# Kernel tuning notes

Hardware: AMD Instinct MI355X
Metric: run time of the kernel (lower is better)

Reference implementation:

```python
import jax, jax.numpy as jnp
import numpy as np

B, D, H, T = 4096, 64, 256, 200

def setup_inputs() -> dict:
    key = jax.random.key(0)
    ks = jax.random.split(key, 4)
    def xavier(k, fan_in, fan_out):
        lim = np.sqrt(6.0 / (fan_in + fan_out)).astype(np.float32)
        return jax.random.uniform(k, (fan_in, fan_out), jnp.float32, -lim, lim)
    return {
        "y0": jax.random.normal(ks[0], (B, D), jnp.float32),
        "t": jnp.arange(T, dtype=jnp.float32) * 0.01,
        "W1": xavier(ks[1], D, H),
        "b1": jnp.zeros((H,), jnp.float32),
        "W2": xavier(ks[2], H, H),
        "b2": jnp.zeros((H,), jnp.float32),
        "W3": xavier(ks[3], H, D),
        "b3": jnp.zeros((D,), jnp.float32),
    }

def reference(y0, t, W1, b1, W2, b2, W3, b3):
    # odeint uses constant dt = t[1] - t[0] (as in the original code)
    dt = t[1] - t[0]
    num_steps = t.shape[0]

    def mlp(y):  # dy/dt = f(y); autonomous, t unused
        h = jax.nn.relu(y @ W1 + b1)
        h = jax.nn.relu(h @ W2 + b2)
        return h @ W3 + b3

    def step(y, _):
        y_new = y + dt * mlp(y)
        return y_new, y_new

    _, ys = jax.lax.scan(step, y0, None, length=num_steps - 1)  # [T-1, B, D]
    # solution: [B, T, D] with solution[:, 0] = y0
    return jnp.concatenate([y0[:, None, :], jnp.transpose(ys, (1, 0, 2))], axis=1)
```

## Files before the change

kernel.cpp:

```cpp
#include <hip/hip_runtime.h>
#include <hip/hip_bf16.h>

#define BATCH   4096
#define DIM     64
#define HID     256
#define TSTEPS  200
#define SROWS   16
#define NBLOCKS (BATCH / SROWS)
#define NTH     512

#define HP  264
#define YPB 72

typedef __bf16 bf16_t;
typedef bf16_t bf16x8 __attribute__((ext_vector_type(8)));
typedef bf16_t bf16x2 __attribute__((ext_vector_type(2)));
typedef float  f32x4  __attribute__((ext_vector_type(4)));

__device__ __forceinline__ unsigned short f2bf(float f) {
    unsigned u = __builtin_bit_cast(unsigned, f);
    u += 0x7FFFu + ((u >> 16) & 1u);
    return (unsigned short)(u >> 16);
}

#if __has_builtin(__builtin_amdgcn_cvt_pk_bf16_f32)
__device__ __forceinline__ unsigned pk2(float lo, float hi) {
    return __builtin_bit_cast(unsigned, __builtin_amdgcn_cvt_pk_bf16_f32(lo, hi));
}
#else
__device__ __forceinline__ unsigned pk2(float lo, float hi) {
    return (unsigned)f2bf(lo) | ((unsigned)f2bf(hi) << 16);
}
#endif

__global__ void prep_weights(const float* __restrict__ W1,
                             const float* __restrict__ W2,
                             const float* __restrict__ W3,
                             unsigned short* __restrict__ ws) {
    int u = blockIdx.x * blockDim.x + threadIdx.x;
    if (u >= 12288) return;
    const int lane = u & 63, l16 = lane & 15, quad = lane >> 4;
    const float* src; int ld, m, k;
    if (u < 2048) {
        int r = u >> 6; int kk = r & 1; int mt = r >> 1;
        src = W1; ld = 256; m = mt * 16 + l16; k = kk * 32 + quad * 8;
    } else if (u < 10240) {
        int r = (u - 2048) >> 6; int kk = r & 7; int mt = r >> 3;
        src = W2; ld = 256; m = mt * 16 + l16; k = kk * 32 + quad * 8;
    } else {
        int r = (u - 10240) >> 6; int kk = r & 7; int mt = r >> 3;
        src = W3; ld = 64;  m = mt * 16 + l16; k = kk * 32 + quad * 8;
    }
    unsigned short tmp[8] __attribute__((aligned(16)));
    #pragma unroll
    for (int j = 0; j < 8; ++j)
        tmp[j] = f2bf(src[(size_t)(k + j) * ld + m]);
    *(uint4*)(ws + (size_t)u * 8) = *(const uint4*)tmp;
}

__global__ void __launch_bounds__(NTH, 2)
ode_kernel(const float* __restrict__ y0,
           const float* __restrict__ tarr,
           const float* __restrict__ b1,
           const float* __restrict__ b2,
           const float* __restrict__ b3,
           const unsigned short* __restrict__ wf,
           float* __restrict__ out) {
    __shared__ __align__(16) unsigned short ybt[SROWS * YPB];
    __shared__ __align__(16) unsigned short h1s[SROWS * HP];
    __shared__ __align__(16) unsigned short h2s[SROWS * HP];

    const int tid  = threadIdx.x;
    const int w    = tid >> 6;
    const int lane = tid & 63;
    const int l16  = lane & 15;
    const int quad = lane >> 4;
    const int b0   = blockIdx.x * SROWS;

    const float dt = tarr[1] - tarr[0];

    const bf16x8* wv = (const bf16x8*)wf;
    bf16x8 w1f[2][2], w2f[2][8], w3f[8];
    #pragma unroll
    for (int mt = 0; mt < 2; ++mt) {
        const int g = w * 2 + mt;
        #pragma unroll
        for (int kk = 0; kk < 2; ++kk) w1f[mt][kk] = wv[(g * 2 + kk) * 64 + lane];
        #pragma unroll
        for (int kk = 0; kk < 8; ++kk) w2f[mt][kk] = wv[2048 + (g * 8 + kk) * 64 + lane];
    }
    if (w < 4)
        #pragma unroll
        for (int kk = 0; kk < 8; ++kk) w3f[kk] = wv[10240 + (w * 8 + kk) * 64 + lane];

    f32x4 binit1[2], binit2[2], binit3;
    #pragma unroll
    for (int mt = 0; mt < 2; ++mt)
        #pragma unroll
        for (int r = 0; r < 4; ++r) {
            binit1[mt][r] = b1[w * 32 + mt * 16 + quad * 4 + r];
            binit2[mt][r] = b2[w * 32 + mt * 16 + quad * 4 + r];
        }

    float yreg[4];
    float* outp = out;
    if (w < 4) {
        #pragma unroll
        for (int r = 0; r < 4; ++r) binit3[r] = b3[w * 16 + quad * 4 + r];
        outp = out + (size_t)(b0 + l16) * (TSTEPS * DIM) + w * 16 + quad * 4;
        float4 v = *(const float4*)&y0[(size_t)(b0 + l16) * DIM + w * 16 + quad * 4];
        yreg[0] = v.x; yreg[1] = v.y; yreg[2] = v.z; yreg[3] = v.w;
        uint2 p; p.x = pk2(v.x, v.y); p.y = pk2(v.z, v.w);
        *(uint2*)&ybt[l16 * YPB + w * 16 + quad * 4] = p;
        *(float4*)outp = v;
        outp += DIM;
    }
    __syncthreads();

    const unsigned short* ybase  = &ybt[l16 * YPB];
    const unsigned short* h1base = &h1s[l16 * HP];
    const unsigned short* h2base = &h2s[l16 * HP];
    const int ep_off = l16 * HP + w * 32 + quad * 4;

    for (int t = 1; t < TSTEPS; ++t) {
        {
            f32x4 acc[2] = {binit1[0], binit1[1]};
            bf16x8 bfr[2];
            #pragma unroll
            for (int kk = 0; kk < 2; ++kk)
                bfr[kk] = *(const bf16x8*)&ybase[kk * 32 + quad * 8];
            #pragma unroll
            for (int kk = 0; kk < 2; ++kk)
                #pragma unroll
                for (int mt = 0; mt < 2; ++mt)
                    acc[mt] = __builtin_amdgcn_mfma_f32_16x16x32_bf16(
                        w1f[mt][kk], bfr[kk], acc[mt], 0, 0, 0);
            #pragma unroll
            for (int mt = 0; mt < 2; ++mt) {
                float v0 = acc[mt][0] > 0.f ? acc[mt][0] : 0.f;
                float v1 = acc[mt][1] > 0.f ? acc[mt][1] : 0.f;
                float v2 = acc[mt][2] > 0.f ? acc[mt][2] : 0.f;
                float v3 = acc[mt][3] > 0.f ? acc[mt][3] : 0.f;
                uint2 p; p.x = pk2(v0, v1); p.y = pk2(v2, v3);
                *(uint2*)&h1s[ep_off + mt * 16] = p;
            }
        }
        __syncthreads();

        {
            f32x4 acc[2] = {binit2[0], binit2[1]};
            bf16x8 bfr[8];
            #pragma unroll
            for (int kk = 0; kk < 8; ++kk)
                bfr[kk] = *(const bf16x8*)&h1base[kk * 32 + quad * 8];
            #pragma unroll
            for (int kk = 0; kk < 8; ++kk)
                #pragma unroll
                for (int mt = 0; mt < 2; ++mt)
                    acc[mt] = __builtin_amdgcn_mfma_f32_16x16x32_bf16(
                        w2f[mt][kk], bfr[kk], acc[mt], 0, 0, 0);
            #pragma unroll
            for (int mt = 0; mt < 2; ++mt) {
                float v0 = acc[mt][0] > 0.f ? acc[mt][0] : 0.f;
                float v1 = acc[mt][1] > 0.f ? acc[mt][1] : 0.f;
                float v2 = acc[mt][2] > 0.f ? acc[mt][2] : 0.f;
                float v3 = acc[mt][3] > 0.f ? acc[mt][3] : 0.f;
                uint2 p; p.x = pk2(v0, v1); p.y = pk2(v2, v3);
                *(uint2*)&h2s[ep_off + mt * 16] = p;
            }
        }
        __syncthreads();

        if (w < 4) {
            f32x4 acc = binit3;
            bf16x8 bfr[8];
            #pragma unroll
            for (int kk = 0; kk < 8; ++kk)
                bfr[kk] = *(const bf16x8*)&h2base[kk * 32 + quad * 8];
            #pragma unroll
            for (int kk = 0; kk < 8; ++kk)
                acc = __builtin_amdgcn_mfma_f32_16x16x32_bf16(
                    w3f[kk], bfr[kk], acc, 0, 0, 0);
            #pragma unroll
            for (int r = 0; r < 4; ++r)
                yreg[r] = __builtin_fmaf(dt, acc[r], yreg[r]);
            uint2 p; p.x = pk2(yreg[0], yreg[1]); p.y = pk2(yreg[2], yreg[3]);
            *(uint2*)&ybt[l16 * YPB + w * 16 + quad * 4] = p;
            float4 ov; ov.x = yreg[0]; ov.y = yreg[1]; ov.z = yreg[2]; ov.w = yreg[3];
            *(float4*)outp = ov;
            outp += DIM;
        }
        __syncthreads();
    }
}

extern "C" void kernel_launch(void* const* d_in, const int* in_sizes, int n_in,
                              void* d_out, int out_size, void* d_ws, size_t ws_size,
                              hipStream_t stream) {
    const float* y0 = (const float*)d_in[0];
    const float* t  = (const float*)d_in[1];
    const float* W1 = (const float*)d_in[2];
    const float* b1 = (const float*)d_in[3];
    const float* W2 = (const float*)d_in[4];
    const float* b2 = (const float*)d_in[5];
    const float* W3 = (const float*)d_in[6];
    const float* b3 = (const float*)d_in[7];
    float* out = (float*)d_out;
    unsigned short* wf = (unsigned short*)d_ws;

    prep_weights<<<48, 256, 0, stream>>>(W1, W2, W3, wf);
    ode_kernel<<<NBLOCKS, NTH, 0, stream>>>(y0, t, b1, b2, b3, wf, out);
}
```

Before: 382.8 us.

## Halve block to 4 waves, each owning 4 M-tiles; split layer-3 accumulation chains

Cuts the block from 8 to 4 wavefronts, so each wave computes four 16-row output tiles per layer instead of two, and all waves take part in layer 3 instead of only half. Layer 3's eight chained MFMAs are split into two independent accumulators to shorten the dependency chain. __syncthreads is replaced by a custom LDS-wait-plus-barrier. The aim is cheaper barriers and better MFMA pipelining per wave. In exchange, register pressure roughly doubles (more weight fragments held in VGPRs), launch bounds drop to 1 block, and fewer waves are resident per CU to hide latency.

```diff
diff --git a/kernel.cpp b/kernel.cpp
--- a/kernel.cpp
+++ b/kernel.cpp
@@ -7,7 +7,7 @@
 #define TSTEPS  200
 #define SROWS   16
 #define NBLOCKS (BATCH / SROWS)
-#define NTH     512
+#define NTH     256
 
 #define HP  264
 #define YPB 72
@@ -32,6 +32,12 @@
     return (unsigned)f2bf(lo) | ((unsigned)f2bf(hi) << 16);
 }
 #endif
+
+__device__ __forceinline__ void bar_lds() {
+    asm volatile("s_waitcnt lgkmcnt(0)" ::: "memory");
+    __builtin_amdgcn_s_barrier();
+    asm volatile("" ::: "memory");
+}
 
 __global__ void prep_weights(const float* __restrict__ W1,
                              const float* __restrict__ W2,
@@ -58,7 +64,7 @@
     *(uint4*)(ws + (size_t)u * 8) = *(const uint4*)tmp;
 }
 
-__global__ void __launch_bounds__(NTH, 2)
+__global__ void __launch_bounds__(NTH, 1)
 ode_kernel(const float* __restrict__ y0,
            const float* __restrict__ tarr,
            const float* __restrict__ b1,
@@ -80,34 +86,32 @@
     const float dt = tarr[1] - tarr[0];
 
     const bf16x8* wv = (const bf16x8*)wf;
-    bf16x8 w1f[2][2], w2f[2][8], w3f[8];
-    #pragma unroll
-    for (int mt = 0; mt < 2; ++mt) {
-        const int g = w * 2 + mt;
+    bf16x8 w1f[4][2], w2f[4][8], w3f[8];
+    #pragma unroll
+    for (int mt = 0; mt < 4; ++mt) {
+        const int g = w * 4 + mt;
         #pragma unroll
         for (int kk = 0; kk < 2; ++kk) w1f[mt][kk] = wv[(g * 2 + kk) * 64 + lane];
         #pragma unroll
         for (int kk = 0; kk < 8; ++kk) w2f[mt][kk] = wv[2048 + (g * 8 + kk) * 64 + lane];
     }
-    if (w < 4)
-        #pragma unroll
-        for (int kk = 0; kk < 8; ++kk) w3f[kk] = wv[10240 + (w * 8 + kk) * 64 + lane];
-
-    f32x4 binit1[2], binit2[2], binit3;
-    #pragma unroll
-    for (int mt = 0; mt < 2; ++mt)
+    #pragma unroll
+    for (int kk = 0; kk < 8; ++kk) w3f[kk] = wv[10240 + (w * 8 + kk) * 64 + lane];
+
+    f32x4 binit1[4], binit2[4], binit3;
+    #pragma unroll
+    for (int mt = 0; mt < 4; ++mt)
         #pragma unroll
         for (int r = 0; r < 4; ++r) {
-            binit1[mt][r] = b1[w * 32 + mt * 16 + quad * 4 + r];
-            binit2[mt][r] = b2[w * 32 + mt * 16 + quad * 4 + r];
-        }
+            binit1[mt][r] = b1[(w * 4 + mt) * 16 + quad * 4 + r];
+            binit2[mt][r] = b2[(w * 4 + mt) * 16 + quad * 4 + r];
+        }
+    #pragma unroll
+    for (int r = 0; r < 4; ++r) binit3[r] = b3[w * 16 + quad * 4 + r];
 
     float yreg[4];
-    float* outp = out;
-    if (w < 4) {
-        #pragma unroll
-        for (int r = 0; r < 4; ++r) binit3[r] = b3[w * 16 + quad * 4 + r];
-        outp = out + (size_t)(b0 + l16) * (TSTEPS * DIM) + w * 16 + quad * 4;
+    float* outp = out + (size_t)(b0 + l16) * (TSTEPS * DIM) + w * 16 + quad * 4;
+    {
         float4 v = *(const float4*)&y0[(size_t)(b0 + l16) * DIM + w * 16 + quad * 4];
         yreg[0] = v.x; yreg[1] = v.y; yreg[2] = v.z; yreg[3] = v.w;
         uint2 p; p.x = pk2(v.x, v.y); p.y = pk2(v.z, v.w);
@@ -115,16 +119,16 @@
         *(float4*)outp = v;
         outp += DIM;
     }
-    __syncthreads();
+    bar_lds();
 
     const unsigned short* ybase  = &ybt[l16 * YPB];
     const unsigned short* h1base = &h1s[l16 * HP];
     const unsigned short* h2base = &h2s[l16 * HP];
-    const int ep_off = l16 * HP + w * 32 + quad * 4;
+    const int ep_off = l16 * HP + w * 64 + quad * 4;
 
     for (int t = 1; t < TSTEPS; ++t) {
         {
-            f32x4 acc[2] = {binit1[0], binit1[1]};
+            f32x4 acc[4] = {binit1[0], binit1[1], binit1[2], binit1[3]};
             bf16x8 bfr[2];
             #pragma unroll
             for (int kk = 0; kk < 2; ++kk)
@@ -132,11 +136,11 @@
             #pragma unroll
             for (int kk = 0; kk < 2; ++kk)
                 #pragma unroll
-                for (int mt = 0; mt < 2; ++mt)
+                for (int mt = 0; mt < 4; ++mt)
                     acc[mt] = __builtin_amdgcn_mfma_f32_16x16x32_bf16(
                         w1f[mt][kk], bfr[kk], acc[mt], 0, 0, 0);
             #pragma unroll
-            for (int mt = 0; mt < 2; ++mt) {
+            for (int mt = 0; mt < 4; ++mt) {
                 float v0 = acc[mt][0] > 0.f ? acc[mt][0] : 0.f;
                 float v1 = acc[mt][1] > 0.f ? acc[mt][1] : 0.f;
                 float v2 = acc[mt][2] > 0.f ? acc[mt][2] : 0.f;
@@ -145,10 +149,10 @@
                 *(uint2*)&h1s[ep_off + mt * 16] = p;
             }
         }
-        __syncthreads();
+        bar_lds();
 
         {
-            f32x4 acc[2] = {binit2[0], binit2[1]};
+            f32x4 acc[4] = {binit2[0], binit2[1], binit2[2], binit2[3]};
             bf16x8 bfr[8];
             #pragma unroll
             for (int kk = 0; kk < 8; ++kk)
@@ -156,11 +160,11 @@
             #pragma unroll
             for (int kk = 0; kk < 8; ++kk)
                 #pragma unroll
-                for (int mt = 0; mt < 2; ++mt)
+                for (int mt = 0; mt < 4; ++mt)
                     acc[mt] = __builtin_amdgcn_mfma_f32_16x16x32_bf16(
                         w2f[mt][kk], bfr[kk], acc[mt], 0, 0, 0);
             #pragma unroll
-            for (int mt = 0; mt < 2; ++mt) {
+            for (int mt = 0; mt < 4; ++mt) {
                 float v0 = acc[mt][0] > 0.f ? acc[mt][0] : 0.f;
                 float v1 = acc[mt][1] > 0.f ? acc[mt][1] : 0.f;
                 float v2 = acc[mt][2] > 0.f ? acc[mt][2] : 0.f;
@@ -169,18 +173,23 @@
                 *(uint2*)&h2s[ep_off + mt * 16] = p;
             }
         }
-        __syncthreads();
-
-        if (w < 4) {
-            f32x4 acc = binit3;
+        bar_lds();
+
+        {
+            f32x4 accA = binit3;
+            f32x4 accB = {0.f, 0.f, 0.f, 0.f};
             bf16x8 bfr[8];
             #pragma unroll
             for (int kk = 0; kk < 8; ++kk)
                 bfr[kk] = *(const bf16x8*)&h2base[kk * 32 + quad * 8];
             #pragma unroll
-            for (int kk = 0; kk < 8; ++kk)
-                acc = __builtin_amdgcn_mfma_f32_16x16x32_bf16(
-                    w3f[kk], bfr[kk], acc, 0, 0, 0);
+            for (int kk = 0; kk < 4; ++kk) {
+                accA = __builtin_amdgcn_mfma_f32_16x16x32_bf16(
+                    w3f[kk], bfr[kk], accA, 0, 0, 0);
+                accB = __builtin_amdgcn_mfma_f32_16x16x32_bf16(
+                    w3f[kk + 4], bfr[kk + 4], accB, 0, 0, 0);
+            }
+            f32x4 acc = accA + accB;
             #pragma unroll
             for (int r = 0; r < 4; ++r)
                 yreg[r] = __builtin_fmaf(dt, acc[r], yreg[r]);
@@ -190,7 +199,7 @@
             *(float4*)outp = ov;
             outp += DIM;
         }
-        __syncthreads();
+        bar_lds();
     }
 }
 
```

After: 421.0 us. 1.1x slower.

## Permute hidden-layer K layout for 16-byte LDS stores, lighter barriers, split MFMA chains

Applied to the files above, without the earlier changes.

Reorders the K index in the packed W2/W3 fragments so each lane's two 4-element MFMA output tiles land contiguously in LDS. This lets the hidden-activation epilogue write one 16-byte store instead of two 8-byte stores. __syncthreads is replaced with an explicit lgkmcnt wait plus s_barrier, which skips waiting on outstanding global stores to the output. The W3 accumulation is split into two independent MFMA chains to cut dependent latency. The cost is a tighter coupling between the weight prep kernel and the main kernel's layout.

```diff
diff --git a/kernel.cpp b/kernel.cpp
--- a/kernel.cpp
+++ b/kernel.cpp
@@ -14,7 +14,6 @@
 
 typedef __bf16 bf16_t;
 typedef bf16_t bf16x8 __attribute__((ext_vector_type(8)));
-typedef bf16_t bf16x2 __attribute__((ext_vector_type(2)));
 typedef float  f32x4  __attribute__((ext_vector_type(4)));
 
 __device__ __forceinline__ unsigned short f2bf(float f) {
@@ -32,6 +31,12 @@
     return (unsigned)f2bf(lo) | ((unsigned)f2bf(hi) << 16);
 }
 #endif
+
+__device__ __forceinline__ void bar_lds() {
+    asm volatile("s_waitcnt lgkmcnt(0)" ::: "memory");
+    __builtin_amdgcn_s_barrier();
+    asm volatile("" ::: "memory");
+}
 
 __global__ void prep_weights(const float* __restrict__ W1,
                              const float* __restrict__ W2,
@@ -40,21 +45,24 @@
     int u = blockIdx.x * blockDim.x + threadIdx.x;
     if (u >= 12288) return;
     const int lane = u & 63, l16 = lane & 15, quad = lane >> 4;
-    const float* src; int ld, m, k;
+    const float* src; int ld, m, kk; bool perm;
     if (u < 2048) {
-        int r = u >> 6; int kk = r & 1; int mt = r >> 1;
-        src = W1; ld = 256; m = mt * 16 + l16; k = kk * 32 + quad * 8;
+        int r = u >> 6; kk = r & 1; int mt = r >> 1;
+        src = W1; ld = 256; m = mt * 16 + l16; perm = false;
     } else if (u < 10240) {
-        int r = (u - 2048) >> 6; int kk = r & 7; int mt = r >> 3;
-        src = W2; ld = 256; m = mt * 16 + l16; k = kk * 32 + quad * 8;
+        int r = (u - 2048) >> 6; kk = r & 7; int mt = r >> 3;
+        src = W2; ld = 256; m = mt * 16 + l16; perm = true;
     } else {
-        int r = (u - 10240) >> 6; int kk = r & 7; int mt = r >> 3;
-        src = W3; ld = 64;  m = mt * 16 + l16; k = kk * 32 + quad * 8;
+        int r = (u - 10240) >> 6; kk = r & 7; int mt = r >> 3;
+        src = W3; ld = 64;  m = mt * 16 + l16; perm = true;
     }
     unsigned short tmp[8] __attribute__((aligned(16)));
     #pragma unroll
-    for (int j = 0; j < 8; ++j)
-        tmp[j] = f2bf(src[(size_t)(k + j) * ld + m]);
+    for (int j = 0; j < 8; ++j) {
+        int k = perm ? kk * 32 + ((j >> 2) << 4) + quad * 4 + (j & 3)
+                     : kk * 32 + quad * 8 + j;
+        tmp[j] = f2bf(src[(size_t)k * ld + m]);
+    }
     *(uint4*)(ws + (size_t)u * 8) = *(const uint4*)tmp;
 }
 
@@ -115,12 +123,12 @@
         *(float4*)outp = v;
         outp += DIM;
     }
-    __syncthreads();
+    bar_lds();
 
     const unsigned short* ybase  = &ybt[l16 * YPB];
     const unsigned short* h1base = &h1s[l16 * HP];
     const unsigned short* h2base = &h2s[l16 * HP];
-    const int ep_off = l16 * HP + w * 32 + quad * 4;
+    const int ep_off = l16 * HP + w * 32 + quad * 8;
 
     for (int t = 1; t < TSTEPS; ++t) {
         {
@@ -135,17 +143,14 @@
                 for (int mt = 0; mt < 2; ++mt)
                     acc[mt] = __builtin_amdgcn_mfma_f32_16x16x32_bf16(
                         w1f[mt][kk], bfr[kk], acc[mt], 0, 0, 0);
-            #pragma unroll
-            for (int mt = 0; mt < 2; ++mt) {
-                float v0 = acc[mt][0] > 0.f ? acc[mt][0] : 0.f;
-                float v1 = acc[mt][1] > 0.f ? acc[mt][1] : 0.f;
-                float v2 = acc[mt][2] > 0.f ? acc[mt][2] : 0.f;
-                float v3 = acc[mt][3] > 0.f ? acc[mt][3] : 0.f;
-                uint2 p; p.x = pk2(v0, v1); p.y = pk2(v2, v3);
-                *(uint2*)&h1s[ep_off + mt * 16] = p;
-            }
-        }
-        __syncthreads();
+            uint4 p;
+            p.x = pk2(acc[0][0] > 0.f ? acc[0][0] : 0.f, acc[0][1] > 0.f ? acc[0][1] : 0.f);
+            p.y = pk2(acc[0][2] > 0.f ? acc[0][2] : 0.f, acc[0][3] > 0.f ? acc[0][3] : 0.f);
+            p.z = pk2(acc[1][0] > 0.f ? acc[1][0] : 0.f, acc[1][1] > 0.f ? acc[1][1] : 0.f);
+            p.w = pk2(acc[1][2] > 0.f ? acc[1][2] : 0.f, acc[1][3] > 0.f ? acc[1][3] : 0.f);
+            *(uint4*)&h1s[ep_off] = p;
+        }
+        bar_lds();
 
         {
             f32x4 acc[2] = {binit2[0], binit2[1]};
@@ -159,28 +164,30 @@
                 for (int mt = 0; mt < 2; ++mt)
                     acc[mt] = __builtin_amdgcn_mfma_f32_16x16x32_bf16(
                         w2f[mt][kk], bfr[kk], acc[mt], 0, 0, 0);
-            #pragma unroll
-            for (int mt = 0; mt < 2; ++mt) {
-                float v0 = acc[mt][0] > 0.f ? acc[mt][0] : 0.f;
-                float v1 = acc[mt][1] > 0.f ? acc[mt][1] : 0.f;
-                float v2 = acc[mt][2] > 0.f ? acc[mt][2] : 0.f;
-                float v3 = acc[mt][3] > 0.f ? acc[mt][3] : 0.f;
-                uint2 p; p.x = pk2(v0, v1); p.y = pk2(v2, v3);
-                *(uint2*)&h2s[ep_off + mt * 16] = p;
-            }
-        }
-        __syncthreads();
+            uint4 p;
+            p.x = pk2(acc[0][0] > 0.f ? acc[0][0] : 0.f, acc[0][1] > 0.f ? acc[0][1] : 0.f);
+            p.y = pk2(acc[0][2] > 0.f ? acc[0][2] : 0.f, acc[0][3] > 0.f ? acc[0][3] : 0.f);
+            p.z = pk2(acc[1][0] > 0.f ? acc[1][0] : 0.f, acc[1][1] > 0.f ? acc[1][1] : 0.f);
+            p.w = pk2(acc[1][2] > 0.f ? acc[1][2] : 0.f, acc[1][3] > 0.f ? acc[1][3] : 0.f);
+            *(uint4*)&h2s[ep_off] = p;
+        }
+        bar_lds();
 
         if (w < 4) {
-            f32x4 acc = binit3;
+            f32x4 accA = binit3;
+            f32x4 accB = {0.f, 0.f, 0.f, 0.f};
             bf16x8 bfr[8];
             #pragma unroll
             for (int kk = 0; kk < 8; ++kk)
                 bfr[kk] = *(const bf16x8*)&h2base[kk * 32 + quad * 8];
             #pragma unroll
-            for (int kk = 0; kk < 8; ++kk)
-                acc = __builtin_amdgcn_mfma_f32_16x16x32_bf16(
-                    w3f[kk], bfr[kk], acc, 0, 0, 0);
+            for (int k = 0; k < 4; ++k) {
+                accA = __builtin_amdgcn_mfma_f32_16x16x32_bf16(
+                    w3f[k], bfr[k], accA, 0, 0, 0);
+                accB = __builtin_amdgcn_mfma_f32_16x16x32_bf16(
+                    w3f[k + 4], bfr[k + 4], accB, 0, 0, 0);
+            }
+            f32x4 acc = accA + accB;
             #pragma unroll
             for (int r = 0; r < 4; ++r)
                 yreg[r] = __builtin_fmaf(dt, acc[r], yreg[r]);
@@ -190,7 +197,7 @@
             *(float4*)outp = ov;
             outp += DIM;
         }
-        __syncthreads();
+        bar_lds();
     }
 }
 
```

Measured after the change: 393.0 us. 1.03x slower.
